# Kernel optimization log

Hardware: AMD Instinct MI355X
Metric: run time of the kernel (lower is better)

The kernel has to match this reference:

```python
import jax, jax.numpy as jnp
import numpy as np

KERNEL_MUL = 2.0
KERNEL_NUM = 5
EPS = 1e-06


def setup_inputs() -> dict:
    key = jax.random.key(0)
    k1, k2 = jax.random.split(key)
    N, D = 4096, 256
    source = jax.random.normal(k1, (N, D), dtype=jnp.float32)
    target = jax.random.normal(k2, (N, D), dtype=jnp.float32)
    return {"source": source, "target": target}


def reference(source, target):
    n_src = source.shape[0]
    total = jnp.concatenate([source, target], axis=0)  # [2N, D]
    n = total.shape[0]
    # the broadcasted (total0 - total1)**2 sum, without the O(N^2*D) tensor).
    sq = jnp.sum(total * total, axis=1)  # [2N]
    L2 = sq[:, None] + sq[None, :] - 2.0 * (total @ total.T)  # [2N, 2N]
    # Bandwidth from detached distances (torch uses L2_distance.data).
    bandwidth = jax.lax.stop_gradient(jnp.sum(L2)) / (n * n - n)
    bandwidth = bandwidth / (KERNEL_MUL ** (KERNEL_NUM // 2))
    kernels = jnp.zeros_like(L2)
    for i in range(KERNEL_NUM):
        bw = bandwidth * (KERNEL_MUL ** i)
        kernels = kernels + jnp.exp(-L2 / (bw + EPS))
    XX = kernels[:n_src, :n_src]
    YY = kernels[n_src:, n_src:]
    XY = kernels[:n_src, n_src:]
    YX = kernels[n_src:, :n_src]
    return jnp.mean(XX + YY - XY - YX)
```

## Files before the change

kernel.cpp:

```cpp
#include <hip/hip_runtime.h>

#define N_TOT 8192
#define NS 4096
#define D 256
#define NB 64
#define NTRI (NB*(NB+1)/2)
#define HALF_B 32

typedef float f32x16 __attribute__((ext_vector_type(16)));
typedef short bf16x8 __attribute__((ext_vector_type(8)));

__device__ __forceinline__ void gload16(const void* g, void* l) {
  __builtin_amdgcn_global_load_lds(
      (const __attribute__((address_space(1))) unsigned int*)g,
      (__attribute__((address_space(3))) unsigned int*)l,
      16, 0, 0);
}

__device__ __forceinline__ unsigned short f2bf(float f) {
  unsigned int u = __builtin_bit_cast(unsigned int, f);
  u += 0x7FFFu + ((u >> 16) & 1u);
  return (unsigned short)(u >> 16);
}

__global__ void k_zero(float* __restrict__ colsum, float* __restrict__ S) {
  colsum[threadIdx.x] = 0.f;
  if (threadIdx.x == 0) S[0] = 0.f;
}

__global__ void k_prep(const float* __restrict__ src, const float* __restrict__ tgt,
                       unsigned short* __restrict__ Xb, float* __restrict__ sqv,
                       float* __restrict__ colsum, float* __restrict__ S) {
  __shared__ float colacc[256];
  __shared__ float wred[4];
  int t = threadIdx.x, l = t & 63, w = t >> 6;
  colacc[t] = 0.f;
  int base = blockIdx.x * 32;
  float c0 = 0.f, c1 = 0.f, c2 = 0.f, c3 = 0.f;
  float wsq = 0.f;
  #pragma unroll
  for (int r = 0; r < 8; ++r) {
    int row = base + w * 8 + r;
    const float* p = (row < NS) ? (src + (size_t)row * D) : (tgt + (size_t)(row - NS) * D);
    float4 v = ((const float4*)p)[l];
    ushort4 bv;
    bv.x = f2bf(v.x); bv.y = f2bf(v.y); bv.z = f2bf(v.z); bv.w = f2bf(v.w);
    ((ushort4*)(Xb + (size_t)row * D))[l] = bv;
    c0 += v.x; c1 += v.y; c2 += v.z; c3 += v.w;
    float s = fmaf(v.x, v.x, fmaf(v.y, v.y, fmaf(v.z, v.z, v.w * v.w)));
    for (int off = 32; off > 0; off >>= 1) s += __shfl_down(s, off, 64);
    if (l == 0) { sqv[row] = s; wsq += s; }
  }
  __syncthreads();
  atomicAdd(&colacc[4 * l + 0], c0);
  atomicAdd(&colacc[4 * l + 1], c1);
  atomicAdd(&colacc[4 * l + 2], c2);
  atomicAdd(&colacc[4 * l + 3], c3);
  if (l == 0) wred[w] = wsq;
  __syncthreads();
  atomicAdd(&colsum[t], colacc[t]);
  if (t == 0) atomicAdd(S, (wred[0] + wred[1]) + (wred[2] + wred[3]));
}

__global__ void k_bw(const float* __restrict__ colsum, const float* __restrict__ S,
                     float* __restrict__ coef) {
  __shared__ double red[256];
  int t = threadIdx.x;
  double c = (double)colsum[t];
  red[t] = c * c;
  __syncthreads();
  for (int s = 128; s > 0; s >>= 1) {
    if (t < s) red[t] += red[t + s];
    __syncthreads();
  }
  if (t == 0) {
    double msq = red[0];
    double Sv = (double)S[0];
    double n = (double)N_TOT;
    double sumL2 = 2.0 * n * Sv - 2.0 * msq;
    double bw = sumL2 / (n * n - n) / 4.0;
    double c4 = 1.0 / (bw * 16.0 + 1e-6);
    coef[0] = (float)(c4 * 1.4426950408889634);
  }
}

__global__ __launch_bounds__(256) void k_main(
    const unsigned short* __restrict__ Xb, const float* __restrict__ sqv,
    const float* __restrict__ coef, float* __restrict__ bpart) {
  int b = blockIdx.x;
  int bi = (int)((2.f * NB + 1.f - sqrtf((float)((2 * NB + 1) * (2 * NB + 1) - 8 * b))) * 0.5f);
  if (bi < 0) bi = 0;
  if (bi > NB - 1) bi = NB - 1;
  while ((bi + 1) * (2 * NB - bi) / 2 <= b) ++bi;
  while (bi * (2 * NB - bi + 1) / 2 > b) --bi;
  int bj = bi + (b - bi * (2 * NB - bi + 1) / 2);

  __shared__ unsigned short ldsA[128 * 64];
  __shared__ unsigned short ldsB[128 * 64];
  __shared__ float sqA[128];
  __shared__ float sqB[128];
  __shared__ float redw[4];

  int t = threadIdx.x;
  int l = t & 63, w = t >> 6;
  int lr = l & 31, half = l >> 5;
  int waveRow = w >> 1, waveCol = w & 1;

  if (t < 128) sqA[t] = sqv[bi * 128 + t];
  else         sqB[t - 128] = sqv[bj * 128 + (t - 128)];
  float A4 = coef[0];

  const unsigned short* arow = Xb + (size_t)bi * 128 * D;
  const unsigned short* brow = Xb + (size_t)bj * 128 * D;

  f32x16 acc[2][2] = {};

  for (int ko = 0; ko < 4; ++ko) {
    if (ko) __syncthreads();
    int kOff = ko * 64;
    #pragma unroll
    for (int p = 0; p < 4; ++p) {
      int seg = p * 256 + w * 64 + l;
      int row = seg >> 3;
      int kb = (seg & 7) ^ (row & 7);
      int goff = row * D + kOff + kb * 8;
      gload16(arow + goff, &ldsA[(p * 4 + w) * 512]);
      gload16(brow + goff, &ldsB[(p * 4 + w) * 512]);
    }
    __syncthreads();
    #pragma unroll
    for (int ks = 0; ks < 4; ++ks) {
      int phys = (2 * ks + half) ^ (lr & 7);
      bf16x8 aF[2], bF[2];
      #pragma unroll
      for (int rb = 0; rb < 2; ++rb) {
        int rowA = waveRow * 64 + rb * 32 + lr;
        aF[rb] = *(const bf16x8*)&ldsA[rowA * 64 + phys * 8];
        int rowB = waveCol * 64 + rb * 32 + lr;
        bF[rb] = *(const bf16x8*)&ldsB[rowB * 64 + phys * 8];
      }
      #pragma unroll
      for (int rb = 0; rb < 2; ++rb)
        #pragma unroll
        for (int cb = 0; cb < 2; ++cb)
          acc[rb][cb] = __builtin_amdgcn_mfma_f32_32x32x16_bf16(aF[rb], bF[cb], acc[rb][cb], 0, 0, 0);
    }
  }

  float lsum = 0.f;
  bool diag = (bi == bj);
  #pragma unroll
  for (int cb = 0; cb < 2; ++cb) {
    int jj = waveCol * 64 + cb * 32 + lr;
    float sqj = sqB[jj];
    #pragma unroll
    for (int rb = 0; rb < 2; ++rb) {
      #pragma unroll
      for (int r = 0; r < 16; ++r) {
        int ii = waveRow * 64 + rb * 32 + (r & 3) + 8 * (r >> 2) + 4 * half;
        float sqi = sqA[ii];
        float dot = acc[rb][cb][r];
        float l2 = fmaf(-2.f, dot, sqi + sqj);
        float e = __builtin_amdgcn_exp2f(-l2 * A4);
        float e2 = e * e, e4 = e2 * e2, e8 = e4 * e4, e16 = e8 * e8;
        float kern = ((e + e2) + (e4 + e8)) + e16;
        if (diag) kern = (ii == jj) ? 0.f : kern;
        lsum += kern;
      }
    }
  }
  for (int off = 32; off > 0; off >>= 1) lsum += __shfl_down(lsum, off, 64);
  if (l == 0) redw[w] = lsum;
  __syncthreads();
  if (t == 0) {
    float tot = (redw[0] + redw[1]) + (redw[2] + redw[3]);
    float wgt = diag ? 1.f : 2.f;
    float sgn = ((bi < HALF_B) == (bj < HALF_B)) ? 1.f : -1.f;
    bpart[b] = tot * wgt * sgn;
  }
}

__global__ void k_final(const float* __restrict__ bpart, float* __restrict__ out) {
  __shared__ double red[256];
  int t = threadIdx.x;
  double s = 0.0;
  for (int k = 0; k < 9; ++k) {
    int idx = k * 256 + t;
    if (idx < NTRI) s += (double)bpart[idx];
  }
  red[t] = s;
  __syncthreads();
  for (int st = 128; st > 0; st >>= 1) {
    if (t < st) red[t] += red[t + st];
    __syncthreads();
  }
  if (t == 0) {
    double total = red[0] + 5.0 * (double)N_TOT;
    out[0] = (float)(total / ((double)NS * (double)NS));
  }
}

extern "C" void kernel_launch(void* const* d_in, const int* in_sizes, int n_in,
                              void* d_out, int out_size, void* d_ws, size_t ws_size,
                              hipStream_t stream) {
  const float* src = (const float*)d_in[0];
  const float* tgt = (const float*)d_in[1];
  float* out = (float*)d_out;
  char* ws = (char*)d_ws;
  unsigned short* Xb = (unsigned short*)ws;
  float* sqv   = (float*)(ws + (4u << 20));
  float* colsum = (float*)(ws + (4u << 20) + (32u << 10));
  float* S     = (float*)(ws + (4u << 20) + (33u << 10));
  float* coef  = (float*)(ws + (4u << 20) + (34u << 10));
  float* bpart = (float*)(ws + (4u << 20) + (35u << 10));

  hipLaunchKernelGGL(k_zero, dim3(1), dim3(256), 0, stream, colsum, S);
  hipLaunchKernelGGL(k_prep, dim3(256), dim3(256), 0, stream, src, tgt, Xb, sqv, colsum, S);
  hipLaunchKernelGGL(k_bw, dim3(1), dim3(256), 0, stream, colsum, S, coef);
  hipLaunchKernelGGL(k_main, dim3(NTRI), dim3(256), 0, stream, Xb, sqv, coef, bpart);
  hipLaunchKernelGGL(k_final, dim3(1), dim3(256), 0, stream, bpart, out);
}
```

Measured before the change: 105.9 us.

## Pre-pack bf16 operands in MFMA fragment layout and fuse final reduction

The prep kernel now writes the bf16 matrix in a layout that matches the MFMA 32x32x16 fragment order, so the main kernel loads operand fragments straight from global memory into registers. This removes the LDS staging and the per-k-step barriers. The zero and final kernels are also removed: column sums are written as per-block partials and reduced in k_bw, and the last k_main block, found through an atomic counter, does the final sum. The trade-off is that operand reuse across waves now depends on L2 and L1 cache hits instead of LDS, and the last-block pattern relies on threadfence ordering.

New measurement: 137.0 us. +29.3%, slower.

```diff
diff --git a/kernel.cpp b/kernel.cpp
--- a/kernel.cpp
+++ b/kernel.cpp
@@ -10,34 +10,22 @@
 typedef float f32x16 __attribute__((ext_vector_type(16)));
 typedef short bf16x8 __attribute__((ext_vector_type(8)));
 
-__device__ __forceinline__ void gload16(const void* g, void* l) {
-  __builtin_amdgcn_global_load_lds(
-      (const __attribute__((address_space(1))) unsigned int*)g,
-      (__attribute__((address_space(3))) unsigned int*)l,
-      16, 0, 0);
-}
-
 __device__ __forceinline__ unsigned short f2bf(float f) {
   unsigned int u = __builtin_bit_cast(unsigned int, f);
   u += 0x7FFFu + ((u >> 16) & 1u);
   return (unsigned short)(u >> 16);
 }
 
-__global__ void k_zero(float* __restrict__ colsum, float* __restrict__ S) {
-  colsum[threadIdx.x] = 0.f;
-  if (threadIdx.x == 0) S[0] = 0.f;
-}
-
 __global__ void k_prep(const float* __restrict__ src, const float* __restrict__ tgt,
-                       unsigned short* __restrict__ Xb, float* __restrict__ sqv,
-                       float* __restrict__ colsum, float* __restrict__ S) {
+                       unsigned short* __restrict__ P, float* __restrict__ sqv,
+                       float* __restrict__ pm) {
   __shared__ float colacc[256];
-  __shared__ float wred[4];
   int t = threadIdx.x, l = t & 63, w = t >> 6;
   colacc[t] = 0.f;
+  __syncthreads();
   int base = blockIdx.x * 32;
+  int chunk = l >> 2, half = (l >> 1) & 1, j0 = (l & 1) * 4;
   float c0 = 0.f, c1 = 0.f, c2 = 0.f, c3 = 0.f;
-  float wsq = 0.f;
   #pragma unroll
   for (int r = 0; r < 8; ++r) {
     int row = base + w * 8 + r;
@@ -45,48 +33,58 @@
     float4 v = ((const float4*)p)[l];
     ushort4 bv;
     bv.x = f2bf(v.x); bv.y = f2bf(v.y); bv.z = f2bf(v.z); bv.w = f2bf(v.w);
-    ((ushort4*)(Xb + (size_t)row * D))[l] = bv;
+    size_t off = (size_t)(row >> 5) * 8192 + chunk * 512 + half * 256 + (row & 31) * 8 + j0;
+    *(ushort4*)(P + off) = bv;
     c0 += v.x; c1 += v.y; c2 += v.z; c3 += v.w;
     float s = fmaf(v.x, v.x, fmaf(v.y, v.y, fmaf(v.z, v.z, v.w * v.w)));
-    for (int off = 32; off > 0; off >>= 1) s += __shfl_down(s, off, 64);
-    if (l == 0) { sqv[row] = s; wsq += s; }
-  }
-  __syncthreads();
+    for (int o = 32; o > 0; o >>= 1) s += __shfl_down(s, o, 64);
+    if (l == 0) sqv[row] = s;
+  }
   atomicAdd(&colacc[4 * l + 0], c0);
   atomicAdd(&colacc[4 * l + 1], c1);
   atomicAdd(&colacc[4 * l + 2], c2);
   atomicAdd(&colacc[4 * l + 3], c3);
-  if (l == 0) wred[w] = wsq;
-  __syncthreads();
-  atomicAdd(&colsum[t], colacc[t]);
-  if (t == 0) atomicAdd(S, (wred[0] + wred[1]) + (wred[2] + wred[3]));
-}
-
-__global__ void k_bw(const float* __restrict__ colsum, const float* __restrict__ S,
-                     float* __restrict__ coef) {
+  __syncthreads();
+  pm[blockIdx.x * 256 + t] = colacc[t];
+}
+
+__global__ void k_bw(const float* __restrict__ pm, const float* __restrict__ sqv,
+                     float* __restrict__ coef, int* __restrict__ cnt) {
   __shared__ double red[256];
   int t = threadIdx.x;
-  double c = (double)colsum[t];
-  red[t] = c * c;
+  float cs = 0.f;
+  for (int b = 0; b < 256; ++b) cs += pm[b * 256 + t];
+  red[t] = (double)cs * (double)cs;
   __syncthreads();
   for (int s = 128; s > 0; s >>= 1) {
     if (t < s) red[t] += red[t + s];
     __syncthreads();
   }
+  double msq = red[0];
+  __syncthreads();
+  double ss = 0.0;
+  for (int k = 0; k < 32; ++k) ss += (double)sqv[t + 256 * k];
+  red[t] = ss;
+  __syncthreads();
+  for (int s = 128; s > 0; s >>= 1) {
+    if (t < s) red[t] += red[t + s];
+    __syncthreads();
+  }
   if (t == 0) {
-    double msq = red[0];
-    double Sv = (double)S[0];
+    double S = red[0];
     double n = (double)N_TOT;
-    double sumL2 = 2.0 * n * Sv - 2.0 * msq;
+    double sumL2 = 2.0 * n * S - 2.0 * msq;
     double bw = sumL2 / (n * n - n) / 4.0;
     double c4 = 1.0 / (bw * 16.0 + 1e-6);
     coef[0] = (float)(c4 * 1.4426950408889634);
+    cnt[0] = 0;
   }
 }
 
 __global__ __launch_bounds__(256) void k_main(
-    const unsigned short* __restrict__ Xb, const float* __restrict__ sqv,
-    const float* __restrict__ coef, float* __restrict__ bpart) {
+    const unsigned short* __restrict__ P, const float* __restrict__ sqv,
+    const float* __restrict__ coef, float* __restrict__ bpart,
+    int* __restrict__ cnt, float* __restrict__ out) {
   int b = blockIdx.x;
   int bi = (int)((2.f * NB + 1.f - sqrtf((float)((2 * NB + 1) * (2 * NB + 1) - 8 * b))) * 0.5f);
   if (bi < 0) bi = 0;
@@ -95,14 +93,12 @@
   while (bi * (2 * NB - bi + 1) / 2 > b) --bi;
   int bj = bi + (b - bi * (2 * NB - bi + 1) / 2);
 
-  __shared__ unsigned short ldsA[128 * 64];
-  __shared__ unsigned short ldsB[128 * 64];
-  __shared__ float sqA[128];
-  __shared__ float sqB[128];
+  __shared__ float sqA[128], sqB[128];
   __shared__ float redw[4];
-
-  int t = threadIdx.x;
-  int l = t & 63, w = t >> 6;
+  __shared__ double red[256];
+  __shared__ int lastFlag;
+
+  int t = threadIdx.x, l = t & 63, w = t >> 6;
   int lr = l & 31, half = l >> 5;
   int waveRow = w >> 1, waveCol = w & 1;
 
@@ -110,41 +106,25 @@
   else         sqB[t - 128] = sqv[bj * 128 + (t - 128)];
   float A4 = coef[0];
 
-  const unsigned short* arow = Xb + (size_t)bi * 128 * D;
-  const unsigned short* brow = Xb + (size_t)bj * 128 * D;
+  const bf16x8* Pf = (const bf16x8*)P;
+  int pa0 = bi * 4 + waveRow * 2;
+  int pb0 = bj * 4 + waveCol * 2;
+  const bf16x8* ap0 = Pf + (size_t)pa0 * 1024 + l;
+  const bf16x8* ap1 = Pf + (size_t)(pa0 + 1) * 1024 + l;
+  const bf16x8* bp0 = Pf + (size_t)pb0 * 1024 + l;
+  const bf16x8* bp1 = Pf + (size_t)(pb0 + 1) * 1024 + l;
 
   f32x16 acc[2][2] = {};
-
-  for (int ko = 0; ko < 4; ++ko) {
-    if (ko) __syncthreads();
-    int kOff = ko * 64;
-    #pragma unroll
-    for (int p = 0; p < 4; ++p) {
-      int seg = p * 256 + w * 64 + l;
-      int row = seg >> 3;
-      int kb = (seg & 7) ^ (row & 7);
-      int goff = row * D + kOff + kb * 8;
-      gload16(arow + goff, &ldsA[(p * 4 + w) * 512]);
-      gload16(brow + goff, &ldsB[(p * 4 + w) * 512]);
-    }
-    __syncthreads();
-    #pragma unroll
-    for (int ks = 0; ks < 4; ++ks) {
-      int phys = (2 * ks + half) ^ (lr & 7);
-      bf16x8 aF[2], bF[2];
-      #pragma unroll
-      for (int rb = 0; rb < 2; ++rb) {
-        int rowA = waveRow * 64 + rb * 32 + lr;
-        aF[rb] = *(const bf16x8*)&ldsA[rowA * 64 + phys * 8];
-        int rowB = waveCol * 64 + rb * 32 + lr;
-        bF[rb] = *(const bf16x8*)&ldsB[rowB * 64 + phys * 8];
-      }
-      #pragma unroll
-      for (int rb = 0; rb < 2; ++rb)
-        #pragma unroll
-        for (int cb = 0; cb < 2; ++cb)
-          acc[rb][cb] = __builtin_amdgcn_mfma_f32_32x32x16_bf16(aF[rb], bF[cb], acc[rb][cb], 0, 0, 0);
-    }
+  #pragma unroll 2
+  for (int c = 0; c < 16; ++c) {
+    bf16x8 aF0 = ap0[c * 64];
+    bf16x8 aF1 = ap1[c * 64];
+    bf16x8 bF0 = bp0[c * 64];
+    bf16x8 bF1 = bp1[c * 64];
+    acc[0][0] = __builtin_amdgcn_mfma_f32_32x32x16_bf16(aF0, bF0, acc[0][0], 0, 0, 0);
+    acc[0][1] = __builtin_amdgcn_mfma_f32_32x32x16_bf16(aF0, bF1, acc[0][1], 0, 0, 0);
+    acc[1][0] = __builtin_amdgcn_mfma_f32_32x32x16_bf16(aF1, bF0, acc[1][0], 0, 0, 0);
+    acc[1][1] = __builtin_amdgcn_mfma_f32_32x32x16_bf16(aF1, bF1, acc[1][1], 0, 0, 0);
   }
 
   float lsum = 0.f;
@@ -169,7 +149,7 @@
       }
     }
   }
-  for (int off = 32; off > 0; off >>= 1) lsum += __shfl_down(lsum, off, 64);
+  for (int o = 32; o > 0; o >>= 1) lsum += __shfl_down(lsum, o, 64);
   if (l == 0) redw[w] = lsum;
   __syncthreads();
   if (t == 0) {
@@ -177,26 +157,28 @@
     float wgt = diag ? 1.f : 2.f;
     float sgn = ((bi < HALF_B) == (bj < HALF_B)) ? 1.f : -1.f;
     bpart[b] = tot * wgt * sgn;
-  }
-}
-
-__global__ void k_final(const float* __restrict__ bpart, float* __restrict__ out) {
-  __shared__ double red[256];
-  int t = threadIdx.x;
-  double s = 0.0;
-  for (int k = 0; k < 9; ++k) {
-    int idx = k * 256 + t;
-    if (idx < NTRI) s += (double)bpart[idx];
-  }
-  red[t] = s;
-  __syncthreads();
-  for (int st = 128; st > 0; st >>= 1) {
-    if (t < st) red[t] += red[t + st];
+    __threadfence();
+    int old = atomicAdd(cnt, 1);
+    lastFlag = (old == NTRI - 1);
+  }
+  __syncthreads();
+  if (lastFlag) {
+    __threadfence();
+    double s = 0.0;
+    for (int k = 0; k < 9; ++k) {
+      int idx = k * 256 + t;
+      if (idx < NTRI) s += (double)bpart[idx];
+    }
+    red[t] = s;
     __syncthreads();
-  }
-  if (t == 0) {
-    double total = red[0] + 5.0 * (double)N_TOT;
-    out[0] = (float)(total / ((double)NS * (double)NS));
+    for (int st = 128; st > 0; st >>= 1) {
+      if (t < st) red[t] += red[t + st];
+      __syncthreads();
+    }
+    if (t == 0) {
+      double total = red[0] + 5.0 * (double)N_TOT;
+      out[0] = (float)(total / ((double)NS * (double)NS));
+    }
   }
 }
 
@@ -207,16 +189,14 @@
   const float* tgt = (const float*)d_in[1];
   float* out = (float*)d_out;
   char* ws = (char*)d_ws;
-  unsigned short* Xb = (unsigned short*)ws;
-  float* sqv   = (float*)(ws + (4u << 20));
-  float* colsum = (float*)(ws + (4u << 20) + (32u << 10));
-  float* S     = (float*)(ws + (4u << 20) + (33u << 10));
-  float* coef  = (float*)(ws + (4u << 20) + (34u << 10));
-  float* bpart = (float*)(ws + (4u << 20) + (35u << 10));
-
-  hipLaunchKernelGGL(k_zero, dim3(1), dim3(256), 0, stream, colsum, S);
-  hipLaunchKernelGGL(k_prep, dim3(256), dim3(256), 0, stream, src, tgt, Xb, sqv, colsum, S);
-  hipLaunchKernelGGL(k_bw, dim3(1), dim3(256), 0, stream, colsum, S, coef);
-  hipLaunchKernelGGL(k_main, dim3(NTRI), dim3(256), 0, stream, Xb, sqv, coef, bpart);
-  hipLaunchKernelGGL(k_final, dim3(1), dim3(256), 0, stream, bpart, out);
-}
+  unsigned short* P = (unsigned short*)ws;
+  float* sqv  = (float*)(ws + (4u << 20));
+  float* pm   = (float*)(ws + (4u << 20) + (32u << 10));
+  float* coef = (float*)(ws + (4u << 20) + (288u << 10));
+  int*   cnt  = (int*)  (ws + (4u << 20) + (288u << 10) + 64);
+  float* bpart = (float*)(ws + (4u << 20) + (289u << 10));
+
+  hipLaunchKernelGGL(k_prep, dim3(256), dim3(256), 0, stream, src, tgt, P, sqv, pm);
+  hipLaunchKernelGGL(k_bw, dim3(1), dim3(256), 0, stream, pm, sqv, coef, cnt);
+  hipLaunchKernelGGL(k_main, dim3(NTRI), dim3(256), 0, stream, P, sqv, coef, bpart, cnt, out);
+}
```

## Fuse final reduction into main kernel via last-block counter; pack epilogue math

Applied to the files above, without the earlier changes.

Removes the separate final reduction kernel. Each main-kernel block now atomically bumps a counter, and whichever block finishes last sums the per-block partials and writes the output. This saves one kernel launch and its dependency gap. The epilogue is also reworked to process element pairs with 2-wide float vectors and a precomputed combined coefficient, aiming for packed FMA/mul instructions. A prep-kernel sync is moved to fix an LDS init race. The cost is an extra atomic and threadfence per block plus added LDS (a 2KB double array) in the main kernel.

Result: slower. 129.6 us (+22.4%).

```diff
diff --git a/kernel.cpp b/kernel.cpp
--- a/kernel.cpp
+++ b/kernel.cpp
@@ -8,6 +8,7 @@
 #define HALF_B 32
 
 typedef float f32x16 __attribute__((ext_vector_type(16)));
+typedef float f32x2 __attribute__((ext_vector_type(2)));
 typedef short bf16x8 __attribute__((ext_vector_type(8)));
 
 __device__ __forceinline__ void gload16(const void* g, void* l) {
@@ -23,9 +24,10 @@
   return (unsigned short)(u >> 16);
 }
 
-__global__ void k_zero(float* __restrict__ colsum, float* __restrict__ S) {
+__global__ void k_zero(float* __restrict__ colsum, float* __restrict__ S,
+                       int* __restrict__ cnt) {
   colsum[threadIdx.x] = 0.f;
-  if (threadIdx.x == 0) S[0] = 0.f;
+  if (threadIdx.x == 0) { S[0] = 0.f; cnt[0] = 0; }
 }
 
 __global__ void k_prep(const float* __restrict__ src, const float* __restrict__ tgt,
@@ -35,6 +37,7 @@
   __shared__ float wred[4];
   int t = threadIdx.x, l = t & 63, w = t >> 6;
   colacc[t] = 0.f;
+  __syncthreads();
   int base = blockIdx.x * 32;
   float c0 = 0.f, c1 = 0.f, c2 = 0.f, c3 = 0.f;
   float wsq = 0.f;
@@ -48,10 +51,9 @@
     ((ushort4*)(Xb + (size_t)row * D))[l] = bv;
     c0 += v.x; c1 += v.y; c2 += v.z; c3 += v.w;
     float s = fmaf(v.x, v.x, fmaf(v.y, v.y, fmaf(v.z, v.z, v.w * v.w)));
-    for (int off = 32; off > 0; off >>= 1) s += __shfl_down(s, off, 64);
+    for (int o = 32; o > 0; o >>= 1) s += __shfl_down(s, o, 64);
     if (l == 0) { sqv[row] = s; wsq += s; }
   }
-  __syncthreads();
   atomicAdd(&colacc[4 * l + 0], c0);
   atomicAdd(&colacc[4 * l + 1], c1);
   atomicAdd(&colacc[4 * l + 2], c2);
@@ -86,7 +88,8 @@
 
 __global__ __launch_bounds__(256) void k_main(
     const unsigned short* __restrict__ Xb, const float* __restrict__ sqv,
-    const float* __restrict__ coef, float* __restrict__ bpart) {
+    const float* __restrict__ coef, float* __restrict__ bpart,
+    int* __restrict__ cnt, float* __restrict__ out) {
   int b = blockIdx.x;
   int bi = (int)((2.f * NB + 1.f - sqrtf((float)((2 * NB + 1) * (2 * NB + 1) - 8 * b))) * 0.5f);
   if (bi < 0) bi = 0;
@@ -97,12 +100,12 @@
 
   __shared__ unsigned short ldsA[128 * 64];
   __shared__ unsigned short ldsB[128 * 64];
-  __shared__ float sqA[128];
-  __shared__ float sqB[128];
+  __shared__ float sqA[128], sqB[128];
   __shared__ float redw[4];
-
-  int t = threadIdx.x;
-  int l = t & 63, w = t >> 6;
+  __shared__ double red[256];
+  __shared__ int lastFlag;
+
+  int t = threadIdx.x, l = t & 63, w = t >> 6;
   int lr = l & 31, half = l >> 5;
   int waveRow = w >> 1, waveCol = w & 1;
 
@@ -147,29 +150,36 @@
     }
   }
 
-  float lsum = 0.f;
+  float c2A4 = 2.f * A4, nA4 = -A4;
+  f32x2 lsum2 = {0.f, 0.f};
   bool diag = (bi == bj);
   #pragma unroll
   for (int cb = 0; cb < 2; ++cb) {
     int jj = waveCol * 64 + cb * 32 + lr;
-    float sqj = sqB[jj];
+    float bjv = nA4 * sqB[jj];
     #pragma unroll
     for (int rb = 0; rb < 2; ++rb) {
       #pragma unroll
-      for (int r = 0; r < 16; ++r) {
+      for (int r = 0; r < 16; r += 2) {
         int ii = waveRow * 64 + rb * 32 + (r & 3) + 8 * (r >> 2) + 4 * half;
-        float sqi = sqA[ii];
-        float dot = acc[rb][cb][r];
-        float l2 = fmaf(-2.f, dot, sqi + sqj);
-        float e = __builtin_amdgcn_exp2f(-l2 * A4);
-        float e2 = e * e, e4 = e2 * e2, e8 = e4 * e4, e16 = e8 * e8;
-        float kern = ((e + e2) + (e4 + e8)) + e16;
-        if (diag) kern = (ii == jj) ? 0.f : kern;
-        lsum += kern;
+        f32x2 dot2 = {acc[rb][cb][r], acc[rb][cb][r + 1]};
+        f32x2 sq2 = {sqA[ii], sqA[ii + 1]};
+        f32x2 tt = c2A4 * dot2 + (nA4 * sq2 + bjv);
+        f32x2 e;
+        e.x = __builtin_amdgcn_exp2f(tt.x);
+        e.y = __builtin_amdgcn_exp2f(tt.y);
+        f32x2 e2 = e * e, e4 = e2 * e2, e8 = e4 * e4, e16 = e8 * e8;
+        f32x2 kern = ((e + e2) + (e4 + e8)) + e16;
+        if (diag) {
+          if (ii == jj) kern.x = 0.f;
+          if (ii + 1 == jj) kern.y = 0.f;
+        }
+        lsum2 += kern;
       }
     }
   }
-  for (int off = 32; off > 0; off >>= 1) lsum += __shfl_down(lsum, off, 64);
+  float lsum = lsum2.x + lsum2.y;
+  for (int o = 32; o > 0; o >>= 1) lsum += __shfl_down(lsum, o, 64);
   if (l == 0) redw[w] = lsum;
   __syncthreads();
   if (t == 0) {
@@ -177,26 +187,28 @@
     float wgt = diag ? 1.f : 2.f;
     float sgn = ((bi < HALF_B) == (bj < HALF_B)) ? 1.f : -1.f;
     bpart[b] = tot * wgt * sgn;
-  }
-}
-
-__global__ void k_final(const float* __restrict__ bpart, float* __restrict__ out) {
-  __shared__ double red[256];
-  int t = threadIdx.x;
-  double s = 0.0;
-  for (int k = 0; k < 9; ++k) {
-    int idx = k * 256 + t;
-    if (idx < NTRI) s += (double)bpart[idx];
-  }
-  red[t] = s;
-  __syncthreads();
-  for (int st = 128; st > 0; st >>= 1) {
-    if (t < st) red[t] += red[t + st];
+    __threadfence();
+    int old = atomicAdd(cnt, 1);
+    lastFlag = (old == NTRI - 1);
+  }
+  __syncthreads();
+  if (lastFlag) {
+    __threadfence();
+    double s = 0.0;
+    for (int k = 0; k < 9; ++k) {
+      int idx = k * 256 + t;
+      if (idx < NTRI) s += (double)bpart[idx];
+    }
+    red[t] = s;
     __syncthreads();
-  }
-  if (t == 0) {
-    double total = red[0] + 5.0 * (double)N_TOT;
-    out[0] = (float)(total / ((double)NS * (double)NS));
+    for (int st = 128; st > 0; st >>= 1) {
+      if (t < st) red[t] += red[t + st];
+      __syncthreads();
+    }
+    if (t == 0) {
+      double total = red[0] + 5.0 * (double)N_TOT;
+      out[0] = (float)(total / ((double)NS * (double)NS));
+    }
   }
 }
 
@@ -212,11 +224,11 @@
   float* colsum = (float*)(ws + (4u << 20) + (32u << 10));
   float* S     = (float*)(ws + (4u << 20) + (33u << 10));
   float* coef  = (float*)(ws + (4u << 20) + (34u << 10));
+  int*   cnt   = (int*)  (ws + (4u << 20) + (34u << 10) + 64);
   float* bpart = (float*)(ws + (4u << 20) + (35u << 10));
 
-  hipLaunchKernelGGL(k_zero, dim3(1), dim3(256), 0, stream, colsum, S);
+  hipLaunchKernelGGL(k_zero, dim3(1), dim3(256), 0, stream, colsum, S, cnt);
   hipLaunchKernelGGL(k_prep, dim3(256), dim3(256), 0, stream, src, tgt, Xb, sqv, colsum, S);
   hipLaunchKernelGGL(k_bw, dim3(1), dim3(256), 0, stream, colsum, S, coef);
-  hipLaunchKernelGGL(k_main, dim3(NTRI), dim3(256), 0, stream, Xb, sqv, coef, bpart);
-  hipLaunchKernelGGL(k_final, dim3(1), dim3(256), 0, stream, bpart, out);
-}
+  hipLaunchKernelGGL(k_main, dim3(NTRI), dim3(256), 0, stream, Xb, sqv, coef, bpart, cnt, out);
+}
```
